# Kernel optimization log

Measured on AMD Instinct MI355X. Metric: run time of the kernel, lower is better.

## Reference

```python
import jax, jax.numpy as jnp
import numpy as np

NUM_FIELDS = 64
# itertools.combinations(range(n), 2) order == row-major upper-triangle (k=1)
_IU, _JU = np.triu_indices(NUM_FIELDS, k=1)
_IU = jnp.asarray(_IU)
_JU = jnp.asarray(_JU)


def setup_inputs() -> dict:
    key = jax.random.key(0)
    inputs = jax.random.normal(key, (16384, NUM_FIELDS, 32), dtype=jnp.float32)
    return {"inputs": inputs}


def reference(inputs) -> jnp.ndarray:
    # Gram matrix of field embeddings per sample: [B, F, F]
    gram = jnp.einsum("bfd,bgd->bfg", inputs, inputs)
    # Upper-triangle (i<j) pairs, same order as itertools.combinations: [B, F*(F-1)/2]
    return gram[:, _IU, _JU]
```

## Files before the change

### kernel.cpp

```cpp
#include <hip/hip_runtime.h>

#define NF 64
#define ND 32
#define NPAIR 2016
#define SPW 4

typedef __attribute__((ext_vector_type(8))) short bf16x8;
typedef __attribute__((ext_vector_type(4))) float f32x4;

__global__ __launch_bounds__(256, 4) void ip_gram_mfma(
    const float* __restrict__ in, float* __restrict__ out) {

    __shared__ float obuf[4][NPAIR];

    const int t = threadIdx.x;
    const int w = t >> 6;
    const int l = t & 63;
    const int g = blockIdx.x * 4 + w;
    const int s0 = g * SPW;

    const int q = l >> 4;
    const int m = l & 15;

    const float* src0 = in + (size_t)s0 * (NF * ND) + (q << 3);
    float* __restrict__ ob = obuf[w];

    float4 bufA[8], bufB[8];

    auto LOAD = [&](float4* buf, int k) {
        const float* sp = src0 + k * (NF * ND);
        #pragma unroll
        for (int r = 0; r < 4; ++r) {
            const float* rowp = sp + (r * 16 + m) * ND;
            buf[2 * r]     = ((const float4*)rowp)[0];
            buf[2 * r + 1] = ((const float4*)rowp)[1];
        }
    };

    auto PROCESS = [&](const float4* buf, int k) {
        bf16x8 fhi[4], flo[4];
        #pragma unroll
        for (int r = 0; r < 4; ++r) {
            float xv[8] = {buf[2*r].x, buf[2*r].y, buf[2*r].z, buf[2*r].w,
                           buf[2*r+1].x, buf[2*r+1].y, buf[2*r+1].z, buf[2*r+1].w};
            #pragma unroll
            for (int e = 0; e < 8; ++e) {
                unsigned xb = __builtin_bit_cast(unsigned, xv[e]);
                fhi[r][e] = (short)(xb >> 16);
                float hf = __builtin_bit_cast(float, xb & 0xFFFF0000u);
                float lf = xv[e] - hf;
                flo[r][e] = (short)(__builtin_bit_cast(unsigned, lf) >> 16);
            }
        }
        #pragma unroll
        for (int ti = 0; ti < 4; ++ti) {
            #pragma unroll
            for (int tj = ti; tj < 4; ++tj) {
                f32x4 c = {0.f, 0.f, 0.f, 0.f};
                c = __builtin_amdgcn_mfma_f32_16x16x32_bf16(fhi[ti], fhi[tj], c, 0, 0, 0);
                c = __builtin_amdgcn_mfma_f32_16x16x32_bf16(fhi[ti], flo[tj], c, 0, 0, 0);
                c = __builtin_amdgcn_mfma_f32_16x16x32_bf16(flo[ti], fhi[tj], c, 0, 0, 0);
                int j = tj * 16 + m;
                #pragma unroll
                for (int r = 0; r < 4; ++r) {
                    int i = ti * 16 + (q << 2) + r;
                    if (ti < tj || j > i) {
                        int p = ((i * (127 - i)) >> 1) + j - i - 1;
                        ob[p] = c[r];
                    }
                }
            }
        }
        float4* __restrict__ dst4 = (float4*)(out + (size_t)(s0 + k) * NPAIR);
        const float4* __restrict__ ob4 = (const float4*)ob;
        #pragma unroll
        for (int it = 0; it < 8; ++it) {
            int idx4 = l + (it << 6);
            if (idx4 < NPAIR / 4) {
                dst4[idx4] = ob4[idx4];
            }
        }
    };

    LOAD(bufA, 0);
    LOAD(bufB, 1);
    PROCESS(bufA, 0);
    LOAD(bufA, 2);
    PROCESS(bufB, 1);
    LOAD(bufB, 3);
    PROCESS(bufA, 2);
    PROCESS(bufB, 3);
}

extern "C" void kernel_launch(void* const* d_in, const int* in_sizes, int n_in,
                              void* d_out, int out_size, void* d_ws, size_t ws_size,
                              hipStream_t stream) {
    const float* in = (const float*)d_in[0];
    float* out = (float*)d_out;
    const int nsamples = in_sizes[0] / (NF * ND);
    ip_gram_mfma<<<nsamples / (4 * SPW), 256, 0, stream>>>(in, out);
}
```

Before: 237.9 us.

## Write gram outputs directly to global memory and halve samples per wave

Removes the LDS staging buffer and its coalesced float4 copy-out, storing each MFMA result element straight to global memory at its upper-triangle index. Samples per wave drop from four to two, so the grid doubles and the software-pipelined load/process sequence becomes two upfront loads followed by two process steps. This frees the 32 KB of shared memory per block and its occupancy cap, but the stores become scattered 4-byte writes whose coalescing depends on the triangle index pattern, and there is less intra-wave overlap of loads with compute.

```diff
diff --git a/kernel.cpp b/kernel.cpp
--- a/kernel.cpp
+++ b/kernel.cpp
@@ -3,15 +3,13 @@
 #define NF 64
 #define ND 32
 #define NPAIR 2016
-#define SPW 4
+#define SPW 2
 
 typedef __attribute__((ext_vector_type(8))) short bf16x8;
 typedef __attribute__((ext_vector_type(4))) float f32x4;
 
 __global__ __launch_bounds__(256, 4) void ip_gram_mfma(
     const float* __restrict__ in, float* __restrict__ out) {
-
-    __shared__ float obuf[4][NPAIR];
 
     const int t = threadIdx.x;
     const int w = t >> 6;
@@ -23,19 +21,20 @@
     const int m = l & 15;
 
     const float* src0 = in + (size_t)s0 * (NF * ND) + (q << 3);
-    float* __restrict__ ob = obuf[w];
 
     float4 bufA[8], bufB[8];
-
-    auto LOAD = [&](float4* buf, int k) {
-        const float* sp = src0 + k * (NF * ND);
-        #pragma unroll
-        for (int r = 0; r < 4; ++r) {
-            const float* rowp = sp + (r * 16 + m) * ND;
-            buf[2 * r]     = ((const float4*)rowp)[0];
-            buf[2 * r + 1] = ((const float4*)rowp)[1];
-        }
-    };
+    #pragma unroll
+    for (int r = 0; r < 4; ++r) {
+        const float* rowp = src0 + (r * 16 + m) * ND;
+        bufA[2 * r]     = ((const float4*)rowp)[0];
+        bufA[2 * r + 1] = ((const float4*)rowp)[1];
+    }
+    #pragma unroll
+    for (int r = 0; r < 4; ++r) {
+        const float* rowp = src0 + NF * ND + (r * 16 + m) * ND;
+        bufB[2 * r]     = ((const float4*)rowp)[0];
+        bufB[2 * r + 1] = ((const float4*)rowp)[1];
+    }
 
     auto PROCESS = [&](const float4* buf, int k) {
         bf16x8 fhi[4], flo[4];
@@ -52,6 +51,7 @@
                 flo[r][e] = (short)(__builtin_bit_cast(unsigned, lf) >> 16);
             }
         }
+        float* __restrict__ dst = out + (size_t)(s0 + k) * NPAIR;
         #pragma unroll
         for (int ti = 0; ti < 4; ++ti) {
             #pragma unroll
@@ -66,30 +66,15 @@
                     int i = ti * 16 + (q << 2) + r;
                     if (ti < tj || j > i) {
                         int p = ((i * (127 - i)) >> 1) + j - i - 1;
-                        ob[p] = c[r];
+                        dst[p] = c[r];
                     }
                 }
             }
         }
-        float4* __restrict__ dst4 = (float4*)(out + (size_t)(s0 + k) * NPAIR);
-        const float4* __restrict__ ob4 = (const float4*)ob;
-        #pragma unroll
-        for (int it = 0; it < 8; ++it) {
-            int idx4 = l + (it << 6);
-            if (idx4 < NPAIR / 4) {
-                dst4[idx4] = ob4[idx4];
-            }
-        }
     };
 
-    LOAD(bufA, 0);
-    LOAD(bufB, 1);
     PROCESS(bufA, 0);
-    LOAD(bufA, 2);
     PROCESS(bufB, 1);
-    LOAD(bufB, 3);
-    PROCESS(bufA, 2);
-    PROCESS(bufB, 3);
 }
 
 extern "C" void kernel_launch(void* const* d_in, const int* in_sizes, int n_in,
```

Measured after the change: 244.6 us. +2.8%, slower.
